# Performance work log

Hardware: AMD Instinct MI355X
Metric: run time of the kernel (lower is better)

The kernel has to match this reference:

```python
import jax, jax.numpy as jnp
import numpy as np

NUM_BINS = 256


def setup_inputs() -> dict:
    key = jax.random.key(0)
    x = jax.random.uniform(key, (16, 3, 1024, 1024), dtype=jnp.float32)
    return {"x": x}


def reference(x) -> jnp.ndarray:
    B, C, H, W = x.shape
    # Quantize to NUM_BINS levels (values in [0,1] so truncation == torch .long())
    x_flat = jnp.clip(x, 0.0, 1.0).reshape(B, C, H * W)
    x_q = jnp.clip((x_flat * (NUM_BINS - 1)).astype(jnp.int32), 0, NUM_BINS - 1)
    # Per-(B,C) histogram via a single flat scatter-add: offset each (b,c)
    # slice into its own NUM_BINS-wide segment of one 1-D buffer.
    offsets = (jnp.arange(B * C, dtype=jnp.int32) * NUM_BINS).reshape(B, C, 1)
    flat_idx = (x_q + offsets).reshape(-1)
    hist = jnp.zeros(B * C * NUM_BINS, dtype=jnp.float32).at[flat_idx].add(1.0)
    hist = hist.reshape(B, C, NUM_BINS)
    # CDF, normalized by total count (clamped at 1 to avoid div-by-zero)
    cdf = jnp.cumsum(hist, axis=2)
    cdf = cdf / jnp.maximum(cdf[:, :, -1:], 1.0)
    # Remap each pixel through its channel's CDF
    y_flat = jnp.take_along_axis(cdf, x_q, axis=2)
    return y_flat.reshape(B, C, H, W).astype(x.dtype)
```

## Files before the change

### kernel.cpp

```cpp
#include <hip/hip_runtime.h>

#define NB 256
#define NCH 48
#define HW (1024*1024)
#define WPC (HW / 4)
#define THREADS 256
#define BPC 64
#define N4 (WPC / BPC)
#define NTILE (N4 / (4 * THREADS))

typedef float  nf4 __attribute__((ext_vector_type(4)));
typedef unsigned int nu4 __attribute__((ext_vector_type(4)));


__device__ __forceinline__ int quant255(float v) {
    v = fminf(fmaxf(v, 0.0f), 1.0f);
    int q = (int)(v * 255.0f);
    q = q < 0 ? 0 : q;
    q = q > 255 ? 255 : q;
    return q;
}

__global__ __launch_bounds__(THREADS, 8) void hist_quant_kernel(
    const float* __restrict__ x, unsigned int* __restrict__ ghist,
    unsigned int* __restrict__ q) {
    __shared__ unsigned int lh[4 * NB];
    const int t = threadIdx.x;
    const int w = t >> 6;
    for (int i = t; i < 4 * NB; i += THREADS) lh[i] = 0u;
    __syncthreads();

    const int ch  = blockIdx.x / BPC;
    const int blk = blockIdx.x % BPC;
    const nf4* xp = (const nf4*)x + (size_t)ch * WPC;
    unsigned int* qp = q + (size_t)ch * WPC;
    const int base = blk * N4;

    for (int tile = 0; tile < NTILE; ++tile) {
        const int tb = base + tile * (4 * THREADS);
        unsigned pw[4];
        #pragma unroll
        for (int k = 0; k < 4; ++k) {
            nf4 v = __builtin_nontemporal_load(xp + tb + k * THREADS + t);
            int q0 = quant255(v.x), q1 = quant255(v.y);
            int q2 = quant255(v.z), q3 = quant255(v.w);
            atomicAdd(&lh[w * NB + q0], 1u);
            atomicAdd(&lh[w * NB + q1], 1u);
            atomicAdd(&lh[w * NB + q2], 1u);
            atomicAdd(&lh[w * NB + q3], 1u);
            pw[k] = (unsigned)q0 | ((unsigned)q1 << 8)
                  | ((unsigned)q2 << 16) | ((unsigned)q3 << 24);
        }
        ((uint4*)(qp + tb))[t] = make_uint4(pw[0], pw[1], pw[2], pw[3]);
    }
    __syncthreads();
    unsigned int s = lh[t] + lh[NB + t] + lh[2 * NB + t] + lh[3 * NB + t];
    if (s) atomicAdd(&ghist[ch * NB + t], s);
}

__global__ __launch_bounds__(THREADS, 8) void remap_kernel(
    const unsigned int* __restrict__ q, const unsigned int* __restrict__ ghist,
    float* __restrict__ y) {
    __shared__ float sbuf[NB];
    __shared__ float lut[NB];
    const int t   = threadIdx.x;
    const int ch  = blockIdx.x / BPC;
    const int blk = blockIdx.x % BPC;

    sbuf[t] = (float)ghist[ch * NB + t];
    __syncthreads();
    for (int off = 1; off < NB; off <<= 1) {
        float add = (t >= off) ? sbuf[t - off] : 0.0f;
        __syncthreads();
        sbuf[t] += add;
        __syncthreads();
    }
    float total = sbuf[NB - 1];
    lut[t] = sbuf[t] / fmaxf(total, 1.0f);
    __syncthreads();

    const unsigned int* qp = q + (size_t)ch * WPC;
    nf4*                yp = (nf4*)y + (size_t)ch * WPC;
    const int base = blk * N4;

    for (int tile = 0; tile < NTILE; ++tile) {
        const int tb = base + tile * (4 * THREADS);
        uint4 pk = ((const uint4*)(qp + tb))[t];
        unsigned pw[4] = {pk.x, pk.y, pk.z, pk.w};
        #pragma unroll
        for (int k = 0; k < 4; ++k) {
            unsigned p = pw[k];
            nf4 o;
            o.x = lut[p & 255];
            o.y = lut[(p >> 8) & 255];
            o.z = lut[(p >> 16) & 255];
            o.w = lut[p >> 24];
            __builtin_nontemporal_store(o, yp + tb + k * THREADS + t);
        }
    }
}

extern "C" void kernel_launch(void* const* d_in, const int* in_sizes, int n_in,
                              void* d_out, int out_size, void* d_ws, size_t ws_size,
                              hipStream_t stream) {
    const float* x = (const float*)d_in[0];
    float* y = (float*)d_out;

    unsigned int* ghist = (unsigned int*)d_ws;
    unsigned int* q     = (unsigned int*)((char*)d_ws + 256 * 1024);

    (void)hipMemsetAsync(d_ws, 0, 48 * 1024, stream);

    hist_quant_kernel<<<NCH * BPC, THREADS, 0, stream>>>(x, ghist, q);
    remap_kernel     <<<NCH * BPC, THREADS, 0, stream>>>(q, ghist, y);
}
```

Baseline: 333.6 us.

## Replace global histogram atomics with per-block partials and a separate LUT build kernel

Each histogram block now writes its 256-bin partial to its own workspace slot instead of doing global atomicAdds, which removes the need for the workspace memset. A new small kernel, one block per channel, sums the 64 partials, runs the prefix scan once and writes a normalized LUT to global memory. The remap kernel then only loads that LUT instead of redoing the scan in every block. The cost is an extra kernel launch and a serial 48-block reduction stage between the two heavy passes.

```diff
diff --git a/kernel.cpp b/kernel.cpp
--- a/kernel.cpp
+++ b/kernel.cpp
@@ -10,7 +10,6 @@
 #define NTILE (N4 / (4 * THREADS))
 
 typedef float  nf4 __attribute__((ext_vector_type(4)));
-typedef unsigned int nu4 __attribute__((ext_vector_type(4)));
 
 
 __device__ __forceinline__ int quant255(float v) {
@@ -22,7 +21,7 @@
 }
 
 __global__ __launch_bounds__(THREADS, 8) void hist_quant_kernel(
-    const float* __restrict__ x, unsigned int* __restrict__ ghist,
+    const float* __restrict__ x, unsigned int* __restrict__ part,
     unsigned int* __restrict__ q) {
     __shared__ unsigned int lh[4 * NB];
     const int t = threadIdx.x;
@@ -54,20 +53,23 @@
         ((uint4*)(qp + tb))[t] = make_uint4(pw[0], pw[1], pw[2], pw[3]);
     }
     __syncthreads();
+
     unsigned int s = lh[t] + lh[NB + t] + lh[2 * NB + t] + lh[3 * NB + t];
-    if (s) atomicAdd(&ghist[ch * NB + t], s);
+    part[(size_t)blockIdx.x * NB + t] = s;
 }
 
-__global__ __launch_bounds__(THREADS, 8) void remap_kernel(
-    const unsigned int* __restrict__ q, const unsigned int* __restrict__ ghist,
-    float* __restrict__ y) {
+__global__ __launch_bounds__(THREADS) void lut_build_kernel(
+    const unsigned int* __restrict__ part, float* __restrict__ lutg) {
     __shared__ float sbuf[NB];
-    __shared__ float lut[NB];
-    const int t   = threadIdx.x;
-    const int ch  = blockIdx.x / BPC;
-    const int blk = blockIdx.x % BPC;
+    const int t  = threadIdx.x;
+    const int ch = blockIdx.x;
 
-    sbuf[t] = (float)ghist[ch * NB + t];
+    const unsigned int* pp = part + (size_t)ch * BPC * NB;
+    unsigned int s = 0;
+    #pragma unroll 8
+    for (int b = 0; b < BPC; ++b) s += pp[b * NB + t];
+
+    sbuf[t] = (float)s;
     __syncthreads();
     for (int off = 1; off < NB; off <<= 1) {
         float add = (t >= off) ? sbuf[t - off] : 0.0f;
@@ -76,7 +78,18 @@
         __syncthreads();
     }
     float total = sbuf[NB - 1];
-    lut[t] = sbuf[t] / fmaxf(total, 1.0f);
+    lutg[ch * NB + t] = sbuf[t] / fmaxf(total, 1.0f);
+}
+
+__global__ __launch_bounds__(THREADS, 8) void remap_kernel(
+    const unsigned int* __restrict__ q, const float* __restrict__ lutg,
+    float* __restrict__ y) {
+    __shared__ float lut[NB];
+    const int t   = threadIdx.x;
+    const int ch  = blockIdx.x / BPC;
+    const int blk = blockIdx.x % BPC;
+
+    lut[t] = lutg[ch * NB + t];
     __syncthreads();
 
     const unsigned int* qp = q + (size_t)ch * WPC;
@@ -106,11 +119,11 @@
     const float* x = (const float*)d_in[0];
     float* y = (float*)d_out;
 
-    unsigned int* ghist = (unsigned int*)d_ws;
-    unsigned int* q     = (unsigned int*)((char*)d_ws + 256 * 1024);
+    unsigned int* part = (unsigned int*)d_ws;
+    float*        lutg = (float*)((char*)d_ws + 4  * 1024 * 1024);
+    unsigned int* q    = (unsigned int*)((char*)d_ws + 64 * 1024 * 1024);
 
-    (void)hipMemsetAsync(d_ws, 0, 48 * 1024, stream);
-
-    hist_quant_kernel<<<NCH * BPC, THREADS, 0, stream>>>(x, ghist, q);
-    remap_kernel     <<<NCH * BPC, THREADS, 0, stream>>>(q, ghist, y);
+    hist_quant_kernel<<<NCH * BPC, THREADS, 0, stream>>>(x, part, q);
+    lut_build_kernel <<<NCH,       THREADS, 0, stream>>>(part, lutg);
+    remap_kernel     <<<NCH * BPC, THREADS, 0, stream>>>(q, lutg, y);
 }
```

After: 344.2 us. 1.03x slower.
